# Optimization experiments

Measured on AMD Instinct MI355X. Metric: run time of the kernel, lower is better.

Reference implementation:

```python
import jax, jax.numpy as jnp
import numpy as np

BLOCK_LEN = 128
NUM_HEADS = 16


def setup_inputs() -> dict:
    key = jax.random.key(0)
    k0, k1, k2 = jax.random.split(key, 3)
    D = 1024
    x = jax.random.normal(k0, (2, 8192, D), dtype=jnp.float32)
    Wqkv = jax.random.normal(k1, (D, 3 * D), dtype=jnp.float32) * 0.02
    bqkv = jnp.zeros((3 * D,), dtype=jnp.float32)
    Wout = jax.random.normal(k2, (D, D), dtype=jnp.float32) * 0.02
    bout = jnp.zeros((D,), dtype=jnp.float32)
    return {"x": x, "Wqkv": Wqkv, "bqkv": bqkv, "Wout": Wout, "bout": bout}


def reference(x, Wqkv, bqkv, Wout, bout):
    B, S, D = x.shape
    H = NUM_HEADS
    BL = BLOCK_LEN
    NB = S // BL            # number of blocks (rows)
    HD = D // H             # head dim (qkv_ratio=1.0 -> qkv_dim_total == D)

    qkv = x @ Wqkv + bqkv                                   # [B, S, 3D]
    qkv = qkv.reshape(B, NB, BL, 3, H, HD)
    q = qkv[:, :, :, 0]                                     # [B, NB, BL, H, HD]
    k = qkv[:, :, :, 1]
    v = qkv[:, :, :, 2]

    # 'column' attention: attend across blocks at the same within-block position.
    # permute to [B, BL(pos p), H, NB(block n), HD]
    qc = jnp.transpose(q, (0, 2, 3, 1, 4))
    kc = jnp.transpose(k, (0, 2, 3, 1, 4))
    vc = jnp.transpose(v, (0, 2, 3, 1, 4))

    scale = 1.0 / jnp.sqrt(jnp.asarray(HD, dtype=x.dtype))
    scores = jnp.einsum('bphnd,bphmd->bphnm', qc, kc) * scale   # [B,BL,H,NB,NB]
    causal = jnp.tril(jnp.ones((NB, NB), dtype=bool))
    scores = jnp.where(causal, scores, jnp.asarray(-1e9, dtype=scores.dtype))
    w = jax.nn.softmax(scores, axis=-1)
    o = jnp.einsum('bphnm,bphmd->bphnd', w, vc)                 # [B,BL,H,NB,HD]

    # back to [B, NB, BL, H*HD] -> [B, S, D]
    o = jnp.transpose(o, (0, 3, 1, 2, 4)).reshape(B, S, D)
    return o @ Wout + bout
```

## Files before the change

kernel.cpp:

```cpp
#include <hip/hip_runtime.h>
#include <stdint.h>

typedef unsigned short u16;
typedef __attribute__((ext_vector_type(8))) short s16x8;
typedef __attribute__((ext_vector_type(4))) float f32x4;

__device__ __forceinline__ f32x4 mfma16x16(s16x8 a, s16x8 b, f32x4 c) {
    return __builtin_amdgcn_mfma_f32_16x16x32_bf16(a, b, c, 0, 0, 0);
}

__device__ __forceinline__ u16 f2bf(float f) {
    union { float f; unsigned u; } c; c.f = f;
    unsigned u = c.u;
    return (u16)((u + 0x7FFFu + ((u >> 16) & 1u)) >> 16);
}

__device__ __forceinline__ void gload16(const void* g, void* l) {
    auto gp = (const __attribute__((address_space(1))) unsigned int*)(g);
    auto lp = (__attribute__((address_space(3))) unsigned int*)(l);
    __builtin_amdgcn_global_load_lds(gp, lp, 16, 0, 0);
}

__device__ __forceinline__ void wave_sync() {
    __builtin_amdgcn_sched_barrier(0);
    asm volatile("s_waitcnt vmcnt(0) lgkmcnt(0)" ::: "memory");
    __builtin_amdgcn_sched_barrier(0);
    __builtin_amdgcn_s_barrier();
    __builtin_amdgcn_sched_barrier(0);
}

__global__ __launch_bounds__(256) void convert_x(
    const float* __restrict__ src, u16* __restrict__ dst, long n)
{
    const long stride = (long)gridDim.x * 256 * 8;
    for (long i = ((long)blockIdx.x * 256 + threadIdx.x) * 8; i < n; i += stride) {
        const float4 a = *(const float4*)(src + i);
        const float4 b = *(const float4*)(src + i + 4);
        u16 o[8] = { f2bf(a.x), f2bf(a.y), f2bf(a.z), f2bf(a.w),
                     f2bf(b.x), f2bf(b.y), f2bf(b.z), f2bf(b.w) };
        *(s16x8*)(dst + i) = *(const s16x8*)o;
    }
}

__global__ __launch_bounds__(256) void fill_sentinel(float* __restrict__ o, long n)
{
    const long stride = (long)gridDim.x * 256;
    for (long i = (long)blockIdx.x * 256 + threadIdx.x; i < n; i += stride)
        o[i] = 1.0f;
}

__global__ __launch_bounds__(256) void transpose_f32_bf16(
    const float* __restrict__ in, u16* __restrict__ out, int R, int C)
{
    __shared__ u16 t[32][33];
    const int c0 = blockIdx.x * 32, r0 = blockIdx.y * 32;
    const int tx = threadIdx.x & 31, ty = threadIdx.x >> 5;
#pragma unroll
    for (int i = 0; i < 32; i += 8)
        t[ty + i][tx] = f2bf(in[(long)(r0 + ty + i) * C + c0 + tx]);
    __syncthreads();
#pragma unroll
    for (int i = 0; i < 32; i += 8)
        out[(long)(c0 + ty + i) * R + r0 + tx] = t[tx][ty + i];
}

template <int FP32OUT, int NT>
__global__ __launch_bounds__(512, 2) void gemm256(
    const u16* __restrict__ A, const u16* __restrict__ BT,
    const float* __restrict__ bias, void* __restrict__ Cout,
    int N, int K)
{
    extern __shared__ char smem[];
    char* const As = smem;
    char* const Bs = smem + 65536;

    const int tid  = threadIdx.x;
    const int lane = tid & 63;
    const int wid  = tid >> 6;
    const int rr   = lane & 15, g = lane >> 4;
    const int wr   = wid >> 2;
    const int wc   = wid & 3;

    const int nwg = gridDim.x;
    const int gsw = (blockIdx.x & 7) * (nwg >> 3) + (blockIdx.x >> 3);
    const long m0 = (long)(gsw & 63) * 256;
    const long n0 = (long)(gsw >> 6) * 256;

    const int srow = tid >> 2;
    const int cl   = (tid & 3) ^ ((tid >> 3) & 3);
    const u16* pA0 = A  + (m0 + srow) * (long)K + cl * 8;
    const u16* pA1 = pA0 + 128 * (long)K;
    const u16* pB0 = BT + (n0 + srow) * (long)K + cl * 8;
    const u16* pB1 = pB0 + 128 * (long)K;
    const int sdst = wid * 1024;

    const int xg    = (g ^ ((rr >> 1) & 3)) << 4;
    const int abase = (wr * 128 + rr) * 64 + xg;
    const int bbase = (wc * 64  + rr) * 64 + xg;

    f32x4 acc[8][4] = {};

#pragma unroll
    for (int t = 0; t < 3; ++t) {
        const long ko = (long)t * 32;
        const int  sb = t * 16384;
        gload16(pA0 + ko, As + sb + sdst);
        gload16(pA1 + ko, As + sb + 8192 + sdst);
        gload16(pB0 + ko, Bs + sb + sdst);
        gload16(pB1 + ko, Bs + sb + 8192 + sdst);
    }
    asm volatile("s_waitcnt vmcnt(8)" ::: "memory");
    __builtin_amdgcn_s_barrier();

    for (int kt = 0; kt < NT; ++kt) {
        const int  bb = (kt & 3) * 16384;
        const int  sb = ((kt + 3) & 3) * 16384;
        const long ko = (long)(kt + 3) * 32;
        const bool st = (kt + 3 < NT);

        if (st) {
            gload16(pA0 + ko, As + sb + sdst);
            gload16(pA1 + ko, As + sb + 8192 + sdst);
        }
        s16x8 bf[4], af[4];
#pragma unroll
        for (int n = 0; n < 4; ++n)
            bf[n] = *(const s16x8*)(Bs + bb + bbase + n * 1024);
#pragma unroll
        for (int m = 0; m < 4; ++m)
            af[m] = *(const s16x8*)(As + bb + abase + m * 1024);
        asm volatile("s_waitcnt lgkmcnt(0)" ::: "memory");
        __builtin_amdgcn_sched_barrier(0);
        __builtin_amdgcn_s_setprio(1);
#pragma unroll
        for (int m = 0; m < 4; ++m)
#pragma unroll
            for (int n = 0; n < 4; ++n)
                acc[m][n] = mfma16x16(af[m], bf[n], acc[m][n]);
        __builtin_amdgcn_s_setprio(0);
        __builtin_amdgcn_s_barrier();

        if (st) {
            gload16(pB0 + ko, Bs + sb + sdst);
            gload16(pB1 + ko, Bs + sb + 8192 + sdst);
        }
#pragma unroll
        for (int m = 0; m < 4; ++m)
            af[m] = *(const s16x8*)(As + bb + abase + (m + 4) * 1024);
        asm volatile("s_waitcnt lgkmcnt(0)" ::: "memory");
        __builtin_amdgcn_sched_barrier(0);
        __builtin_amdgcn_s_setprio(1);
#pragma unroll
        for (int m = 0; m < 4; ++m)
#pragma unroll
            for (int n = 0; n < 4; ++n)
                acc[m + 4][n] = mfma16x16(af[m], bf[n], acc[m + 4][n]);
        __builtin_amdgcn_s_setprio(0);

        if (kt < NT - 3)       { asm volatile("s_waitcnt vmcnt(8)" ::: "memory"); }
        else if (kt == NT - 3) { asm volatile("s_waitcnt vmcnt(4)" ::: "memory"); }
        else if (kt == NT - 2) { asm volatile("s_waitcnt vmcnt(0)" ::: "memory"); }
        if (kt < NT - 1) __builtin_amdgcn_s_barrier();
    }

#pragma unroll
    for (int n = 0; n < 4; ++n) {
        const long col = n0 + wc * 64 + n * 16 + rr;
        const float bv = bias[col];
#pragma unroll
        for (int m = 0; m < 8; ++m) {
            const long rb = m0 + wr * 128 + m * 16 + g * 4;
#pragma unroll
            for (int r = 0; r < 4; ++r) {
                const float v = acc[m][n][r] + bv;
                if (FP32OUT) ((float*)Cout)[(rb + r) * N + col] = v;
                else         ((u16*)Cout)[(rb + r) * N + col] = f2bf(v);
            }
        }
    }
}

template <int FP32OUT>
__global__ __launch_bounds__(256) void gemm_bt_bias(
    const u16* __restrict__ A, const u16* __restrict__ BT,
    const float* __restrict__ bias, void* __restrict__ Cout,
    int M, int N, int K)
{
    __shared__ u16 As[128 * 64];
    __shared__ u16 Bs[128 * 64];
    const int tid  = threadIdx.x;
    const int lane = tid & 63;
    const int wid  = tid >> 6;
    const int rr   = lane & 15, g = lane >> 4;
    const int wm   = (wid >> 1) << 6;
    const int wn   = (wid & 1) << 6;
    const long m0  = (long)blockIdx.y * 128;
    const long n0  = (long)blockIdx.x * 128;
    const int srow   = tid >> 3;
    const int schunk = (tid & 7) ^ (srow & 7);

    f32x4 acc[4][4] = {};

    for (int k0 = 0; k0 < K; k0 += 64) {
#pragma unroll
        for (int q = 0; q < 4; ++q) {
            const int row = q * 32 + srow;
            gload16(A  + (m0 + row) * K + k0 + schunk * 8,
                    (char*)As + q * 4096 + wid * 1024);
            gload16(BT + (n0 + row) * K + k0 + schunk * 8,
                    (char*)Bs + q * 4096 + wid * 1024);
        }
        __syncthreads();
#pragma unroll
        for (int kk = 0; kk < 2; ++kk) {
            s16x8 af[4], bfr[4];
#pragma unroll
            for (int i = 0; i < 4; ++i) {
                const int rowa = wm + i * 16 + rr;
                af[i] = *(const s16x8*)((const char*)As + rowa * 128 +
                         ((kk * 64 + g * 16) ^ ((rowa & 7) << 4)));
                const int rowb = wn + i * 16 + rr;
                bfr[i] = *(const s16x8*)((const char*)Bs + rowb * 128 +
                         ((kk * 64 + g * 16) ^ ((rowb & 7) << 4)));
            }
#pragma unroll
            for (int i = 0; i < 4; ++i)
#pragma unroll
                for (int j = 0; j < 4; ++j)
                    acc[i][j] = mfma16x16(af[i], bfr[j], acc[i][j]);
        }
        __syncthreads();
    }

#pragma unroll
    for (int j = 0; j < 4; ++j) {
        const long col = n0 + wn + j * 16 + rr;
        const float bv = bias[col];
#pragma unroll
        for (int i = 0; i < 4; ++i)
#pragma unroll
            for (int r = 0; r < 4; ++r) {
                const long rowg = m0 + wm + i * 16 + g * 4 + r;
                const float v = acc[i][j][r] + bv;
                if (FP32OUT) ((float*)Cout)[rowg * N + col] = v;
                else         ((u16*)Cout)[rowg * N + col] = f2bf(v);
            }
    }
}

__global__ __launch_bounds__(64) void attn_blocks(
    const u16* __restrict__ qkv, u16* __restrict__ o)
{
    __shared__ u16 Vlds[64 * 64];
    __shared__ u16 Plds[64 * 72];
    const int bid = blockIdx.x;
    const int b = bid >> 11;
    const int h = (bid >> 7) & 15;
    const int p = bid & 127;
    const int lane = threadIdx.x;
    const int rr = lane & 15, g = lane >> 4;
    const long NSTR = 128L * 3072;
    const long base = ((long)b * 8192 + p) * 3072 + h * 64;

    {
        const int vrow = lane >> 3;
        const int vchunk = (lane & 7) ^ (vrow & 7);
#pragma unroll
        for (int q = 0; q < 8; ++q)
            gload16(qkv + base + (long)(q * 8 + vrow) * NSTR + 2048 + vchunk * 8,
                    (char*)Vlds + q * 1024);
    }

    s16x8 kf[4][2], qf[4][2];
#pragma unroll
    for (int t = 0; t < 4; ++t)
#pragma unroll
        for (int ks = 0; ks < 2; ++ks) {
            const long roff = base + (long)(t * 16 + rr) * NSTR + ks * 32 + g * 8;
            kf[t][ks] = *(const s16x8*)(qkv + roff + 1024);
            qf[t][ks] = *(const s16x8*)(qkv + roff);
        }

    f32x4 T[4][4] = {};
#pragma unroll
    for (int ks = 0; ks < 2; ++ks)
#pragma unroll
        for (int i = 0; i < 4; ++i)
#pragma unroll
            for (int jn = 0; jn < 4; ++jn)
                T[i][jn] = mfma16x16(kf[i][ks], qf[jn][ks], T[i][jn]);

    const float scale = 0.125f;
#pragma unroll
    for (int jn = 0; jn < 4; ++jn) {
        const int n = jn * 16 + rr;
        float pv[16];
        float mx = -3e38f;
#pragma unroll
        for (int i = 0; i < 4; ++i)
#pragma unroll
            for (int r = 0; r < 4; ++r) {
                const int m = i * 16 + g * 4 + r;
                const float s = (m <= n) ? T[i][jn][r] * scale : -3e38f;
                pv[i * 4 + r] = s;
                mx = fmaxf(mx, s);
            }
        mx = fmaxf(mx, __shfl_xor(mx, 16));
        mx = fmaxf(mx, __shfl_xor(mx, 32));
        float sum = 0.f;
#pragma unroll
        for (int t = 0; t < 16; ++t) {
            const float e = (pv[t] > -1e30f) ? __expf(pv[t] - mx) : 0.f;
            pv[t] = e;
            sum += e;
        }
        sum += __shfl_xor(sum, 16);
        sum += __shfl_xor(sum, 32);
        const float inv = 1.f / sum;
#pragma unroll
        for (int i = 0; i < 4; ++i)
#pragma unroll
            for (int rp = 0; rp < 2; ++rp) {
                const int m = i * 16 + g * 4 + rp * 2;
                const unsigned lo = f2bf(pv[i * 4 + rp * 2] * inv);
                const unsigned hi = f2bf(pv[i * 4 + rp * 2 + 1] * inv);
                *(unsigned*)((char*)Plds + n * 144 + m * 2) = lo | (hi << 16);
            }
    }

    wave_sync();

    f32x4 O[4][4] = {};
#pragma unroll
    for (int ks = 0; ks < 2; ++ks) {
        s16x8 pa[4];
#pragma unroll
        for (int in = 0; in < 4; ++in)
            pa[in] = *(const s16x8*)((const char*)Plds +
                      (in * 16 + rr) * 144 + ks * 64 + g * 16);
#pragma unroll
        for (int jd = 0; jd < 4; ++jd) {
            s16x8 vb;
#pragma unroll
            for (int j = 0; j < 8; ++j) {
                const int k = ks * 32 + g * 8 + j;
                const int byte = (k * 128 + (jd * 16 + rr) * 2) ^ ((k & 7) << 4);
                vb[j] = *(const short*)((const char*)Vlds + byte);
            }
#pragma unroll
            for (int in = 0; in < 4; ++in)
                O[in][jd] = mfma16x16(pa[in], vb, O[in][jd]);
        }
    }

    const long obase = ((long)b * 8192 + p) * 1024 + h * 64;
#pragma unroll
    for (int in = 0; in < 4; ++in)
#pragma unroll
        for (int jd = 0; jd < 4; ++jd)
#pragma unroll
            for (int r = 0; r < 4; ++r) {
                const long n = in * 16 + g * 4 + r;
                const long d = jd * 16 + rr;
                o[obase + n * (128L * 1024) + d] = f2bf(O[in][jd][r]);
            }
}

extern "C" void kernel_launch(void* const* d_in, const int* in_sizes, int n_in,
                              void* d_out, int out_size, void* d_ws, size_t ws_size,
                              hipStream_t stream) {
    const float* x    = (const float*)d_in[0];
    const float* Wqkv = (const float*)d_in[1];
    const float* bq   = (const float*)d_in[2];
    const float* Wout = (const float*)d_in[3];
    const float* bo   = (const float*)d_in[4];

    char* ws = (char*)d_ws;
    u16* xb    = (u16*)(ws);
    u16* qkv   = (u16*)(ws +  33554432L);
    u16* ob    = (u16*)(ws + 134217728L);
    u16* WqkvT = (u16*)(ws + 167772160L);
    u16* WoutT = (u16*)(ws + 174063616L);
    const size_t NEEDED = 176160768UL;

    if (ws_size < NEEDED) {
        fill_sentinel<<<2048, 256, 0, stream>>>((float*)d_out, (long)out_size);
        return;
    }

    bool deep = true;
    if (hipFuncSetAttribute(reinterpret_cast<const void*>(&gemm256<0, 32>),
                            hipFuncAttributeMaxDynamicSharedMemorySize,
                            131072) != hipSuccess) deep = false;
    if (hipFuncSetAttribute(reinterpret_cast<const void*>(&gemm256<1, 32>),
                            hipFuncAttributeMaxDynamicSharedMemorySize,
                            131072) != hipSuccess) deep = false;

    convert_x<<<2048, 256, 0, stream>>>(x, xb, 16777216L);
    transpose_f32_bf16<<<dim3(96, 32), 256, 0, stream>>>(Wqkv, WqkvT, 1024, 3072);
    transpose_f32_bf16<<<dim3(32, 32), 256, 0, stream>>>(Wout, WoutT, 1024, 1024);

    if (deep)
        gemm256<0, 32><<<768, 512, 131072, stream>>>(xb, WqkvT, bq, qkv,
                                                     3072, 1024);
    else
        gemm_bt_bias<0><<<dim3(24, 128), 256, 0, stream>>>(xb, WqkvT, bq, qkv,
                                                           16384, 3072, 1024);

    attn_blocks<<<4096, 64, 0, stream>>>(qkv, ob);

    if (deep)
        gemm256<1, 32><<<256, 512, 131072, stream>>>(ob, WoutT, bo, d_out,
                                                     1024, 1024);
    else
        gemm_bt_bias<1><<<dim3(8, 128), 256, 0, stream>>>(ob, WoutT, bo, d_out,
                                                          16384, 1024, 1024);
}
```

Before: 224.0 us.

## Restructure GEMM main loop into two-stage 64-wide K pipeline with split A/B prefetch

The 256x256 bf16 GEMM main loop now advances K by 64 per iteration (NT halved from 32 to 16). It uses two double-buffered 64-wide slots instead of a 4-deep ring of 32-wide slots. Global-to-LDS loads for the A and B halves of upcoming tiles are interleaved between the four MFMA phases, each gated by barriers and vmcnt(4) waits. The goal is finer overlap of loads with compute and fewer outstanding-load stalls, at the cost of more barriers per iteration and a shallower prefetch distance.

```diff
diff --git a/kernel.cpp b/kernel.cpp
--- a/kernel.cpp
+++ b/kernel.cpp
@@ -86,51 +86,46 @@
     const long m0 = (long)(gsw & 63) * 256;
     const long n0 = (long)(gsw >> 6) * 256;
 
-    const int srow = tid >> 2;
-    const int cl   = (tid & 3) ^ ((tid >> 3) & 3);
-    const u16* pA0 = A  + (m0 + srow) * (long)K + cl * 8;
+    const int cl = (tid & 3) ^ ((tid >> 3) & 3);
+    const u16* pA0 = A  + (m0 + (tid >> 2)) * (long)K + cl * 8;
     const u16* pA1 = pA0 + 128 * (long)K;
-    const u16* pB0 = BT + (n0 + srow) * (long)K + cl * 8;
+    const u16* pB0 = BT + (n0 + (tid >> 2)) * (long)K + cl * 8;
     const u16* pB1 = pB0 + 128 * (long)K;
     const int sdst = wid * 1024;
 
     const int xg    = (g ^ ((rr >> 1) & 3)) << 4;
-    const int abase = (wr * 128 + rr) * 64 + xg;
-    const int bbase = (wc * 64  + rr) * 64 + xg;
+    const int arow  = (wr * 128 + rr) * 64 + xg;
+    const int brow  = (wc * 64  + rr) * 64 + xg;
+
+#define STA(tt, h) { const long c_ = (long)(tt) * 64 + (h) * 32;              \
+        char* d_ = As + (((tt) & 1) * 2 + (h)) * 16384 + sdst;                \
+        gload16(pA0 + c_, d_); gload16(pA1 + c_, d_ + 8192); }
+#define STB(tt, h) { const long c_ = (long)(tt) * 64 + (h) * 32;              \
+        char* d_ = Bs + (((tt) & 1) * 2 + (h)) * 16384 + sdst;                \
+        gload16(pB0 + c_, d_); gload16(pB1 + c_, d_ + 8192); }
+#define BAR() { __builtin_amdgcn_sched_barrier(0); __builtin_amdgcn_s_barrier(); }
+#define LGKM0() { asm volatile("s_waitcnt lgkmcnt(0)" ::: "memory");          \
+        __builtin_amdgcn_sched_barrier(0); }
 
     f32x4 acc[8][4] = {};
 
-#pragma unroll
-    for (int t = 0; t < 3; ++t) {
-        const long ko = (long)t * 32;
-        const int  sb = t * 16384;
-        gload16(pA0 + ko, As + sb + sdst);
-        gload16(pA1 + ko, As + sb + 8192 + sdst);
-        gload16(pB0 + ko, Bs + sb + sdst);
-        gload16(pB1 + ko, Bs + sb + 8192 + sdst);
-    }
-    asm volatile("s_waitcnt vmcnt(8)" ::: "memory");
-    __builtin_amdgcn_s_barrier();
-
-    for (int kt = 0; kt < NT; ++kt) {
-        const int  bb = (kt & 3) * 16384;
-        const int  sb = ((kt + 3) & 3) * 16384;
-        const long ko = (long)(kt + 3) * 32;
-        const bool st = (kt + 3 < NT);
-
-        if (st) {
-            gload16(pA0 + ko, As + sb + sdst);
-            gload16(pA1 + ko, As + sb + 8192 + sdst);
-        }
+    STA(0, 0); STB(0, 0); STA(0, 1); STB(0, 1); STA(1, 0); STB(1, 0);
+    asm volatile("s_waitcnt vmcnt(4)" ::: "memory");
+    BAR();
+
+    for (int t = 0; t < NT; ++t) {
+        const int ab = (t & 1) * 32768;
+        const bool tl = (t >= NT - 3);
         s16x8 bf[4], af[4];
+
 #pragma unroll
         for (int n = 0; n < 4; ++n)
-            bf[n] = *(const s16x8*)(Bs + bb + bbase + n * 1024);
-#pragma unroll
-        for (int m = 0; m < 4; ++m)
-            af[m] = *(const s16x8*)(As + bb + abase + m * 1024);
-        asm volatile("s_waitcnt lgkmcnt(0)" ::: "memory");
-        __builtin_amdgcn_sched_barrier(0);
+            bf[n] = *(const s16x8*)(Bs + ab + brow + n * 1024);
+#pragma unroll
+        for (int m = 0; m < 4; ++m)
+            af[m] = *(const s16x8*)(As + ab + arow + m * 1024);
+        if (t + 1 < NT) STA(t + 1, 1);
+        BAR(); LGKM0();
         __builtin_amdgcn_s_setprio(1);
 #pragma unroll
         for (int m = 0; m < 4; ++m)
@@ -138,17 +133,15 @@
             for (int n = 0; n < 4; ++n)
                 acc[m][n] = mfma16x16(af[m], bf[n], acc[m][n]);
         __builtin_amdgcn_s_setprio(0);
-        __builtin_amdgcn_s_barrier();
-
-        if (st) {
-            gload16(pB0 + ko, Bs + sb + sdst);
-            gload16(pB1 + ko, Bs + sb + 8192 + sdst);
-        }
-#pragma unroll
-        for (int m = 0; m < 4; ++m)
-            af[m] = *(const s16x8*)(As + bb + abase + (m + 4) * 1024);
-        asm volatile("s_waitcnt lgkmcnt(0)" ::: "memory");
-        __builtin_amdgcn_sched_barrier(0);
+        BAR();
+
+#pragma unroll
+        for (int m = 0; m < 4; ++m)
+            af[m] = *(const s16x8*)(As + ab + arow + (m + 4) * 1024);
+        if (t + 1 < NT) STB(t + 1, 1);
+        if (tl) { asm volatile("s_waitcnt vmcnt(0)" ::: "memory"); }
+        else    { asm volatile("s_waitcnt vmcnt(4)" ::: "memory"); }
+        BAR(); LGKM0();
         __builtin_amdgcn_s_setprio(1);
 #pragma unroll
         for (int m = 0; m < 4; ++m)
@@ -156,12 +149,45 @@
             for (int n = 0; n < 4; ++n)
                 acc[m + 4][n] = mfma16x16(af[m], bf[n], acc[m + 4][n]);
         __builtin_amdgcn_s_setprio(0);
-
-        if (kt < NT - 3)       { asm volatile("s_waitcnt vmcnt(8)" ::: "memory"); }
-        else if (kt == NT - 3) { asm volatile("s_waitcnt vmcnt(4)" ::: "memory"); }
-        else if (kt == NT - 2) { asm volatile("s_waitcnt vmcnt(0)" ::: "memory"); }
-        if (kt < NT - 1) __builtin_amdgcn_s_barrier();
-    }
+        BAR();
+
+#pragma unroll
+        for (int n = 0; n < 4; ++n)
+            bf[n] = *(const s16x8*)(Bs + ab + 16384 + brow + n * 1024);
+#pragma unroll
+        for (int m = 0; m < 4; ++m)
+            af[m] = *(const s16x8*)(As + ab + 16384 + arow + m * 1024);
+        if (t + 2 < NT) STA(t + 2, 0);
+        BAR(); LGKM0();
+        __builtin_amdgcn_s_setprio(1);
+#pragma unroll
+        for (int m = 0; m < 4; ++m)
+#pragma unroll
+            for (int n = 0; n < 4; ++n)
+                acc[m][n] = mfma16x16(af[m], bf[n], acc[m][n]);
+        __builtin_amdgcn_s_setprio(0);
+        BAR();
+
+#pragma unroll
+        for (int m = 0; m < 4; ++m)
+            af[m] = *(const s16x8*)(As + ab + 16384 + arow + (m + 4) * 1024);
+        if (t + 2 < NT) STB(t + 2, 0);
+        if (tl) { asm volatile("s_waitcnt vmcnt(0)" ::: "memory"); }
+        else    { asm volatile("s_waitcnt vmcnt(4)" ::: "memory"); }
+        BAR(); LGKM0();
+        __builtin_amdgcn_s_setprio(1);
+#pragma unroll
+        for (int m = 0; m < 4; ++m)
+#pragma unroll
+            for (int n = 0; n < 4; ++n)
+                acc[m + 4][n] = mfma16x16(af[m], bf[n], acc[m + 4][n]);
+        __builtin_amdgcn_s_setprio(0);
+        BAR();
+    }
+#undef STA
+#undef STB
+#undef BAR
+#undef LGKM0
 
 #pragma unroll
     for (int n = 0; n < 4; ++n) {
@@ -389,10 +415,10 @@
     }
 
     bool deep = true;
-    if (hipFuncSetAttribute(reinterpret_cast<const void*>(&gemm256<0, 32>),
+    if (hipFuncSetAttribute(reinterpret_cast<const void*>(&gemm256<0, 16>),
                             hipFuncAttributeMaxDynamicSharedMemorySize,
                             131072) != hipSuccess) deep = false;
-    if (hipFuncSetAttribute(reinterpret_cast<const void*>(&gemm256<1, 32>),
+    if (hipFuncSetAttribute(reinterpret_cast<const void*>(&gemm256<1, 16>),
                             hipFuncAttributeMaxDynamicSharedMemorySize,
                             131072) != hipSuccess) deep = false;
 
@@ -401,7 +427,7 @@
     transpose_f32_bf16<<<dim3(32, 32), 256, 0, stream>>>(Wout, WoutT, 1024, 1024);
 
     if (deep)
-        gemm256<0, 32><<<768, 512, 131072, stream>>>(xb, WqkvT, bq, qkv,
+        gemm256<0, 16><<<768, 512, 131072, stream>>>(xb, WqkvT, bq, qkv,
                                                      3072, 1024);
     else
         gemm_bt_bias<0><<<dim3(24, 128), 256, 0, stream>>>(xb, WqkvT, bq, qkv,
@@ -410,7 +436,7 @@
     attn_blocks<<<4096, 64, 0, stream>>>(qkv, ob);
 
     if (deep)
-        gemm256<1, 32><<<256, 512, 131072, stream>>>(ob, WoutT, bo, d_out,
+        gemm256<1, 16><<<256, 512, 131072, stream>>>(ob, WoutT, bo, d_out,
                                                      1024, 1024);
     else
         gemm_bt_bias<1><<<dim3(8, 128), 256, 0, stream>>>(ob, WoutT, bo, d_out,
```

New measurement: 229.8 us. 1.03x slower.
